# Kernel tuning notes

Measured on AMD Instinct MI355X. Metric: run time of the kernel, lower is better.

## Reference

```python
import jax, jax.numpy as jnp
import numpy as np

B, N, DIM, H, DH = 2, 2048, 256, 4, 32


def setup_inputs() -> dict:
    key = jax.random.key(0)
    k0, k1, k2, k3, k4 = jax.random.split(key, 5)
    x = jax.random.normal(k0, (B, N, DIM), dtype=jnp.float32)
    pos_bias = jax.random.normal(k1, (H, N, N), dtype=jnp.float32) * 0.02
    focus_present_mask = jax.random.randint(k2, (B,), 0, 2).astype(bool)
    W_qkv = jax.random.normal(k3, (DIM, 3 * H * DH), dtype=jnp.float32) * 0.05
    W_out = jax.random.normal(k4, (H * DH, DIM), dtype=jnp.float32) * 0.05
    return {"x": x, "pos_bias": pos_bias, "focus_present_mask": focus_present_mask,
            "W_qkv": W_qkv, "W_out": W_out}


def reference(x, pos_bias, focus_present_mask, W_qkv, W_out):
    b, n, _ = x.shape
    scale = DH ** -0.5
    qkv = x @ W_qkv                                  # [b, n, 3*h*dh]
    q, k, v = jnp.split(qkv, 3, axis=-1)
    split_heads = lambda t: t.reshape(b, n, H, DH).transpose(0, 2, 1, 3)  # b h n d
    q, k, v = split_heads(q), split_heads(k), split_heads(v)
    q = q * scale
    sim = jnp.einsum('bhid,bhjd->bhij', q, k)        # [b, h, n, n]
    sim = sim + pos_bias[None]                       # additive relative-position bias
    # focus-present masking: batches with mask=True attend only to self (eye),
    # batches with mask=False attend everywhere -> always-apply form is equivalent.
    eye = jnp.eye(n, dtype=bool)
    mask = jnp.where(focus_present_mask[:, None, None, None], eye[None, None], True)
    neg = -jnp.finfo(sim.dtype).max
    sim = jnp.where(mask, sim, neg)
    sim = sim - jax.lax.stop_gradient(sim.max(axis=-1, keepdims=True))
    attn = jax.nn.softmax(sim, axis=-1)
    out = jnp.einsum('bhij,bhjd->bhid', attn, v)     # [b, h, n, d]
    out = out.transpose(0, 2, 1, 3).reshape(b, n, H * DH)
    return out @ W_out
```

## Files before the change

kernel.cpp:

```cpp
#include <hip/hip_runtime.h>
#include <hip/hip_bf16.h>

#define DEVI __device__ __forceinline__

typedef short bf16x8 __attribute__((ext_vector_type(8)));
typedef float f32x4 __attribute__((ext_vector_type(4)));
typedef unsigned short u16x4 __attribute__((ext_vector_type(4)));

static constexpr int B_ = 2, N_ = 2048, DIM_ = 256, H_ = 4, DH_ = 32;
static constexpr int NQKV_ = 3 * H_ * DH_;
static constexpr float SCALE_ = 0.17677669529663687f;

DEVI unsigned short f2bf(float f) {
  __hip_bfloat16 h = __float2bfloat16(f);
  return *reinterpret_cast<unsigned short*>(&h);
}

__global__ void k_convert(const float* __restrict__ x, const float* __restrict__ Wqkv,
                          const float* __restrict__ Wout,
                          unsigned short* __restrict__ xb,
                          unsigned short* __restrict__ wqkvt,
                          unsigned short* __restrict__ woutt) {
  const int tid = blockIdx.x * blockDim.x + threadIdx.x;
  const int nt = gridDim.x * blockDim.x;
  for (int i = tid; i < B_ * N_ * DIM_; i += nt) xb[i] = f2bf(x[i]);
  for (int i = tid; i < NQKV_ * 256; i += nt)
    wqkvt[i] = f2bf(Wqkv[(i & 255) * NQKV_ + (i >> 8)]);
  for (int i = tid; i < 256 * 128; i += nt)
    woutt[i] = f2bf(Wout[(i & 127) * 256 + (i >> 7)]);
}

__global__ __launch_bounds__(256) void k_gemm_qkv(
    const unsigned short* __restrict__ A,
    const unsigned short* __restrict__ Bt,
    unsigned short* __restrict__ Qo,
    unsigned short* __restrict__ Ko,
    unsigned short* __restrict__ Vo,
    unsigned short* __restrict__ Vto) {
  const int tid = threadIdx.x;
  const int w = tid >> 6, l = tid & 63;
  const int lr = l & 15, g = l >> 4;
  const int row0 = blockIdx.x * 64 + (w >> 1) * 32;
  const int col0 = blockIdx.y * 64 + (w & 1) * 32;
  f32x4 acc[2][2] = {};
#pragma unroll
  for (int kb = 0; kb < 256; kb += 32) {
    bf16x8 a0 = *(const bf16x8*)(A + (row0 + lr) * 256 + kb + g * 8);
    bf16x8 a1 = *(const bf16x8*)(A + (row0 + 16 + lr) * 256 + kb + g * 8);
    bf16x8 b0 = *(const bf16x8*)(Bt + (col0 + lr) * 256 + kb + g * 8);
    bf16x8 b1 = *(const bf16x8*)(Bt + (col0 + 16 + lr) * 256 + kb + g * 8);
    acc[0][0] = __builtin_amdgcn_mfma_f32_16x16x32_bf16(a0, b0, acc[0][0], 0, 0, 0);
    acc[0][1] = __builtin_amdgcn_mfma_f32_16x16x32_bf16(a0, b1, acc[0][1], 0, 0, 0);
    acc[1][0] = __builtin_amdgcn_mfma_f32_16x16x32_bf16(a1, b0, acc[1][0], 0, 0, 0);
    acc[1][1] = __builtin_amdgcn_mfma_f32_16x16x32_bf16(a1, b1, acc[1][1], 0, 0, 0);
  }
#pragma unroll
  for (int mi = 0; mi < 2; mi++)
#pragma unroll
    for (int ni = 0; ni < 2; ni++) {
      const int colg = col0 + ni * 16 + lr;
      const int sec = colg >> 7;
      const int h = (colg >> 5) & 3;
      const int d = colg & 31;
      const int rbase = row0 + mi * 16 + g * 4;
      const int bb = rbase >> 11;
      const int n0 = rbase & (N_ - 1);
      if (sec == 0) {
#pragma unroll
        for (int r = 0; r < 4; r++)
          Qo[((bb * H_ + h) * N_ + n0 + r) * DH_ + d] = f2bf(acc[mi][ni][r] * SCALE_);
      } else if (sec == 1) {
#pragma unroll
        for (int r = 0; r < 4; r++)
          Ko[((bb * H_ + h) * N_ + n0 + r) * DH_ + d] = f2bf(acc[mi][ni][r]);
      } else {
        u16x4 vp;
#pragma unroll
        for (int r = 0; r < 4; r++) {
          const unsigned short vb = f2bf(acc[mi][ni][r]);
          Vo[((bb * H_ + h) * N_ + n0 + r) * DH_ + d] = vb;
          vp[r] = vb;
        }
        const int c32 = n0 & ~31;
        const int local = n0 & 31;
        const int slot = ((local & 15) >> 2) * 8 + ((local >> 4) << 2);
        *(u16x4*)(Vto + ((bb * H_ + h) * DH_ + d) * N_ + c32 + slot) = vp;
      }
    }
}

__global__ __launch_bounds__(512) void k_attn_lds(
    const unsigned short* __restrict__ Q,
    const unsigned short* __restrict__ K,
    const unsigned short* __restrict__ Vt,
    const unsigned short* __restrict__ V,
    const float* __restrict__ bias,
    const int* __restrict__ mask,
    unsigned short* __restrict__ AO) {
  const int bh = blockIdx.y;
  const int b = bh >> 2, h = bh & 3;
  const int qt = blockIdx.x;
  const int tid = threadIdx.x;
  const int qb = qt * 16;
  if (mask[b] != 0) {
    if (tid < 64) {
      const int q = tid >> 2;
      const int d8 = (tid & 3) * 8;
      bf16x8 v = *(const bf16x8*)(V + ((size_t)bh * N_ + qb + q) * DH_ + d8);
      *(bf16x8*)(AO + (size_t)(b * N_ + qb + q) * (H_ * DH_) + h * DH_ + d8) = v;
    }
    return;
  }
  __shared__ float so[16][8][32];
  __shared__ float ss[16][8];
  const int w = tid >> 6, l = tid & 63, lr = l & 15, g = l >> 4;
  const int c0 = w * 256;
  const unsigned short* Kp = K + bh * N_ * DH_;
  const unsigned short* Vtp = Vt + bh * DH_ * N_;
  const float* biasrow = bias + (size_t)(h * N_ + qb + lr) * N_;
  const bf16x8 qf = *(const bf16x8*)(Q + (bh * N_ + qb + lr) * DH_ + g * 8);
  float s = 0.f;
  f32x4 o0 = {}, o1 = {};
  for (int c = c0; c < c0 + 256; c += 32) {
    bf16x8 k0 = *(const bf16x8*)(Kp + (c + lr) * DH_ + g * 8);
    bf16x8 k1 = *(const bf16x8*)(Kp + (c + 16 + lr) * DH_ + g * 8);
    f32x4 z = {};
    f32x4 st0 = __builtin_amdgcn_mfma_f32_16x16x32_bf16(k0, qf, z, 0, 0, 0);
    f32x4 st1 = __builtin_amdgcn_mfma_f32_16x16x32_bf16(k1, qf, z, 0, 0, 0);
    f32x4 bi0 = *(const f32x4*)(biasrow + c + g * 4);
    f32x4 bi1 = *(const f32x4*)(biasrow + c + 16 + g * 4);
    bf16x8 pf;
#pragma unroll
    for (int r = 0; r < 4; r++) {
      const float p0 = __expf(st0[r] + bi0[r]);
      const float p1 = __expf(st1[r] + bi1[r]);
      s += p0 + p1;
      pf[r] = (short)f2bf(p0);
      pf[4 + r] = (short)f2bf(p1);
    }
    bf16x8 v0 = *(const bf16x8*)(Vtp + lr * N_ + c + g * 8);
    bf16x8 v1 = *(const bf16x8*)(Vtp + (16 + lr) * N_ + c + g * 8);
    o0 = __builtin_amdgcn_mfma_f32_16x16x32_bf16(v0, pf, o0, 0, 0, 0);
    o1 = __builtin_amdgcn_mfma_f32_16x16x32_bf16(v1, pf, o1, 0, 0, 0);
  }
  s += __shfl_xor(s, 16);
  s += __shfl_xor(s, 32);
  *(f32x4*)&so[lr][w][g * 4] = o0;
  *(f32x4*)&so[lr][w][16 + g * 4] = o1;
  if (g == 0) ss[lr][w] = s;
  __syncthreads();
  {
    const int q = tid >> 5;
    const int d = tid & 31;
    float acc = 0.f, ssum = 0.f;
#pragma unroll
    for (int w2 = 0; w2 < 8; w2++) {
      acc += so[q][w2][d];
      ssum += ss[q][w2];
    }
    AO[(size_t)(b * N_ + qb + q) * (H_ * DH_) + h * DH_ + d] = f2bf(acc / ssum);
  }
}

__global__ __launch_bounds__(256) void k_gemm_out(
    const unsigned short* __restrict__ A,
    const unsigned short* __restrict__ Bt,
    float* __restrict__ out) {
  const int tid = threadIdx.x;
  const int w = tid >> 6, l = tid & 63;
  const int lr = l & 15, g = l >> 4;
  const int row0 = blockIdx.x * 64 + (w >> 1) * 32;
  const int col0 = blockIdx.y * 64 + (w & 1) * 32;
  f32x4 acc[2][2] = {};
#pragma unroll
  for (int kb = 0; kb < 128; kb += 32) {
    bf16x8 a0 = *(const bf16x8*)(A + (row0 + lr) * 128 + kb + g * 8);
    bf16x8 a1 = *(const bf16x8*)(A + (row0 + 16 + lr) * 128 + kb + g * 8);
    bf16x8 b0 = *(const bf16x8*)(Bt + (col0 + lr) * 128 + kb + g * 8);
    bf16x8 b1 = *(const bf16x8*)(Bt + (col0 + 16 + lr) * 128 + kb + g * 8);
    acc[0][0] = __builtin_amdgcn_mfma_f32_16x16x32_bf16(a0, b0, acc[0][0], 0, 0, 0);
    acc[0][1] = __builtin_amdgcn_mfma_f32_16x16x32_bf16(a0, b1, acc[0][1], 0, 0, 0);
    acc[1][0] = __builtin_amdgcn_mfma_f32_16x16x32_bf16(a1, b0, acc[1][0], 0, 0, 0);
    acc[1][1] = __builtin_amdgcn_mfma_f32_16x16x32_bf16(a1, b1, acc[1][1], 0, 0, 0);
  }
#pragma unroll
  for (int mi = 0; mi < 2; mi++)
#pragma unroll
    for (int ni = 0; ni < 2; ni++) {
      const int colg = col0 + ni * 16 + lr;
      const int rbase = row0 + mi * 16 + g * 4;
#pragma unroll
      for (int r = 0; r < 4; r++)
        out[(size_t)(rbase + r) * 256 + colg] = acc[mi][ni][r];
    }
}

extern "C" void kernel_launch(void* const* d_in, const int* in_sizes, int n_in,
                              void* d_out, int out_size, void* d_ws, size_t ws_size,
                              hipStream_t stream) {
  const float* x = (const float*)d_in[0];
  const float* bias = (const float*)d_in[1];
  const int* mask = (const int*)d_in[2];
  const float* Wqkv = (const float*)d_in[3];
  const float* Wout = (const float*)d_in[4];
  float* out = (float*)d_out;
  char* ws = (char*)d_ws;

  unsigned short* xb    = (unsigned short*)(ws + 0);
  unsigned short* wqkvt = (unsigned short*)(ws + 2097152);
  unsigned short* woutt = (unsigned short*)(ws + 2293760);
  unsigned short* Qb    = (unsigned short*)(ws + 2359296);
  unsigned short* Kb    = (unsigned short*)(ws + 3407872);
  unsigned short* Vb    = (unsigned short*)(ws + 4456448);
  unsigned short* Vtb   = (unsigned short*)(ws + 5505024);
  unsigned short* AOb   = (unsigned short*)(ws + 6553600);

  k_convert<<<dim3(1024), dim3(256), 0, stream>>>(x, Wqkv, Wout, xb, wqkvt, woutt);
  k_gemm_qkv<<<dim3(64, 6), dim3(256), 0, stream>>>(xb, wqkvt, Qb, Kb, Vb, Vtb);
  k_attn_lds<<<dim3(128, B_ * H_), dim3(512), 0, stream>>>(
      Qb, Kb, Vtb, Vb, bias, mask, AOb);
  k_gemm_out<<<dim3(64, 4), dim3(256), 0, stream>>>(AOb, woutt, out);
}
```

Before: 45.18 us.

## Fuse fp32-to-bf16 conversion into QKV and output GEMM kernels

Removes the separate conversion kernel and instead converts x to bf16 in registers inside the QKV GEMM, while each GEMM block transposes and converts its weight tile into padded LDS. This saves one kernel launch and the round trip of writing and re-reading bf16 copies. In exchange, every block redundantly converts its weight slice, and the QKV GEMM reads fp32 x, which is twice the bytes of bf16.

```diff
diff --git a/kernel.cpp b/kernel.cpp
--- a/kernel.cpp
+++ b/kernel.cpp
@@ -16,39 +16,47 @@
   return *reinterpret_cast<unsigned short*>(&h);
 }
 
-__global__ void k_convert(const float* __restrict__ x, const float* __restrict__ Wqkv,
-                          const float* __restrict__ Wout,
-                          unsigned short* __restrict__ xb,
-                          unsigned short* __restrict__ wqkvt,
-                          unsigned short* __restrict__ woutt) {
-  const int tid = blockIdx.x * blockDim.x + threadIdx.x;
-  const int nt = gridDim.x * blockDim.x;
-  for (int i = tid; i < B_ * N_ * DIM_; i += nt) xb[i] = f2bf(x[i]);
-  for (int i = tid; i < NQKV_ * 256; i += nt)
-    wqkvt[i] = f2bf(Wqkv[(i & 255) * NQKV_ + (i >> 8)]);
-  for (int i = tid; i < 256 * 128; i += nt)
-    woutt[i] = f2bf(Wout[(i & 127) * 256 + (i >> 7)]);
-}
-
 __global__ __launch_bounds__(256) void k_gemm_qkv(
-    const unsigned short* __restrict__ A,
-    const unsigned short* __restrict__ Bt,
+    const float* __restrict__ X,
+    const float* __restrict__ Wqkv,
     unsigned short* __restrict__ Qo,
     unsigned short* __restrict__ Ko,
     unsigned short* __restrict__ Vo,
     unsigned short* __restrict__ Vto) {
+  constexpr int LDB = 258;
+  __shared__ unsigned short Bts[64 * LDB];
   const int tid = threadIdx.x;
+  const int col0b = blockIdx.y * 64;
+  for (int p = tid; p < 64 * 256; p += 256) {
+    const int col = p & 63;
+    const int k = p >> 6;
+    Bts[col * LDB + k] = f2bf(Wqkv[k * NQKV_ + col0b + col]);
+  }
+  __syncthreads();
+
   const int w = tid >> 6, l = tid & 63;
   const int lr = l & 15, g = l >> 4;
   const int row0 = blockIdx.x * 64 + (w >> 1) * 32;
-  const int col0 = blockIdx.y * 64 + (w & 1) * 32;
+  const int colw = (w & 1) * 32;
+  const float* xr0 = X + (size_t)(row0 + lr) * 256;
+  const float* xr1 = X + (size_t)(row0 + 16 + lr) * 256;
   f32x4 acc[2][2] = {};
 #pragma unroll
   for (int kb = 0; kb < 256; kb += 32) {
-    bf16x8 a0 = *(const bf16x8*)(A + (row0 + lr) * 256 + kb + g * 8);
-    bf16x8 a1 = *(const bf16x8*)(A + (row0 + 16 + lr) * 256 + kb + g * 8);
-    bf16x8 b0 = *(const bf16x8*)(Bt + (col0 + lr) * 256 + kb + g * 8);
-    bf16x8 b1 = *(const bf16x8*)(Bt + (col0 + 16 + lr) * 256 + kb + g * 8);
+    f32x4 xa = *(const f32x4*)(xr0 + kb + g * 8);
+    f32x4 xb4 = *(const f32x4*)(xr0 + kb + g * 8 + 4);
+    f32x4 xc = *(const f32x4*)(xr1 + kb + g * 8);
+    f32x4 xd = *(const f32x4*)(xr1 + kb + g * 8 + 4);
+    bf16x8 a0, a1;
+#pragma unroll
+    for (int j = 0; j < 4; j++) {
+      a0[j] = (short)f2bf(xa[j]);
+      a0[4 + j] = (short)f2bf(xb4[j]);
+      a1[j] = (short)f2bf(xc[j]);
+      a1[4 + j] = (short)f2bf(xd[j]);
+    }
+    bf16x8 b0 = *(const bf16x8*)(&Bts[(colw + lr) * LDB + kb + g * 8]);
+    bf16x8 b1 = *(const bf16x8*)(&Bts[(colw + 16 + lr) * LDB + kb + g * 8]);
     acc[0][0] = __builtin_amdgcn_mfma_f32_16x16x32_bf16(a0, b0, acc[0][0], 0, 0, 0);
     acc[0][1] = __builtin_amdgcn_mfma_f32_16x16x32_bf16(a0, b1, acc[0][1], 0, 0, 0);
     acc[1][0] = __builtin_amdgcn_mfma_f32_16x16x32_bf16(a1, b0, acc[1][0], 0, 0, 0);
@@ -58,7 +66,7 @@
   for (int mi = 0; mi < 2; mi++)
 #pragma unroll
     for (int ni = 0; ni < 2; ni++) {
-      const int colg = col0 + ni * 16 + lr;
+      const int colg = col0b + colw + ni * 16 + lr;
       const int sec = colg >> 7;
       const int h = (colg >> 5) & 3;
       const int d = colg & 31;
@@ -164,20 +172,30 @@
 
 __global__ __launch_bounds__(256) void k_gemm_out(
     const unsigned short* __restrict__ A,
-    const unsigned short* __restrict__ Bt,
+    const float* __restrict__ Wout,
     float* __restrict__ out) {
+  constexpr int LDB = 130;
+  __shared__ unsigned short Bts[64 * LDB];
   const int tid = threadIdx.x;
+  const int col0b = blockIdx.y * 64;
+  for (int p = tid; p < 64 * 128; p += 256) {
+    const int col = p & 63;
+    const int k = p >> 6;
+    Bts[col * LDB + k] = f2bf(Wout[k * 256 + col0b + col]);
+  }
+  __syncthreads();
+
   const int w = tid >> 6, l = tid & 63;
   const int lr = l & 15, g = l >> 4;
   const int row0 = blockIdx.x * 64 + (w >> 1) * 32;
-  const int col0 = blockIdx.y * 64 + (w & 1) * 32;
+  const int colw = (w & 1) * 32;
   f32x4 acc[2][2] = {};
 #pragma unroll
   for (int kb = 0; kb < 128; kb += 32) {
     bf16x8 a0 = *(const bf16x8*)(A + (row0 + lr) * 128 + kb + g * 8);
     bf16x8 a1 = *(const bf16x8*)(A + (row0 + 16 + lr) * 128 + kb + g * 8);
-    bf16x8 b0 = *(const bf16x8*)(Bt + (col0 + lr) * 128 + kb + g * 8);
-    bf16x8 b1 = *(const bf16x8*)(Bt + (col0 + 16 + lr) * 128 + kb + g * 8);
+    bf16x8 b0 = *(const bf16x8*)(&Bts[(colw + lr) * LDB + kb + g * 8]);
+    bf16x8 b1 = *(const bf16x8*)(&Bts[(colw + 16 + lr) * LDB + kb + g * 8]);
     acc[0][0] = __builtin_amdgcn_mfma_f32_16x16x32_bf16(a0, b0, acc[0][0], 0, 0, 0);
     acc[0][1] = __builtin_amdgcn_mfma_f32_16x16x32_bf16(a0, b1, acc[0][1], 0, 0, 0);
     acc[1][0] = __builtin_amdgcn_mfma_f32_16x16x32_bf16(a1, b0, acc[1][0], 0, 0, 0);
@@ -187,7 +205,7 @@
   for (int mi = 0; mi < 2; mi++)
 #pragma unroll
     for (int ni = 0; ni < 2; ni++) {
-      const int colg = col0 + ni * 16 + lr;
+      const int colg = col0b + colw + ni * 16 + lr;
       const int rbase = row0 + mi * 16 + g * 4;
 #pragma unroll
       for (int r = 0; r < 4; r++)
@@ -206,18 +224,14 @@
   float* out = (float*)d_out;
   char* ws = (char*)d_ws;
 
-  unsigned short* xb    = (unsigned short*)(ws + 0);
-  unsigned short* wqkvt = (unsigned short*)(ws + 2097152);
-  unsigned short* woutt = (unsigned short*)(ws + 2293760);
-  unsigned short* Qb    = (unsigned short*)(ws + 2359296);
-  unsigned short* Kb    = (unsigned short*)(ws + 3407872);
-  unsigned short* Vb    = (unsigned short*)(ws + 4456448);
-  unsigned short* Vtb   = (unsigned short*)(ws + 5505024);
-  unsigned short* AOb   = (unsigned short*)(ws + 6553600);
-
-  k_convert<<<dim3(1024), dim3(256), 0, stream>>>(x, Wqkv, Wout, xb, wqkvt, woutt);
-  k_gemm_qkv<<<dim3(64, 6), dim3(256), 0, stream>>>(xb, wqkvt, Qb, Kb, Vb, Vtb);
+  unsigned short* Qb    = (unsigned short*)(ws + 0);
+  unsigned short* Kb    = (unsigned short*)(ws + 1048576);
+  unsigned short* Vb    = (unsigned short*)(ws + 2097152);
+  unsigned short* Vtb   = (unsigned short*)(ws + 3145728);
+  unsigned short* AOb   = (unsigned short*)(ws + 4194304);
+
+  k_gemm_qkv<<<dim3(64, 6), dim3(256), 0, stream>>>(x, Wqkv, Qb, Kb, Vb, Vtb);
   k_attn_lds<<<dim3(128, B_ * H_), dim3(512), 0, stream>>>(
       Qb, Kb, Vtb, Vb, bias, mask, AOb);
-  k_gemm_out<<<dim3(64, 4), dim3(256), 0, stream>>>(AOb, woutt, out);
-}
+  k_gemm_out<<<dim3(64, 4), dim3(256), 0, stream>>>(AOb, Wout, out);
+}
```

Result: no change. 45.04 us (-0.3%).
